# Kernel optimization log

Measured on AMD Instinct MI355X. Metric: run time of the kernel, lower is better.

The kernel has to match this reference:

```python
import jax, jax.numpy as jnp
import numpy as np

N, E, D, EH, EF, NT, OUT = 100000, 320000, 32, 32, 16, 100, 3
NUM_STEPS = 3


def setup_inputs() -> dict:
    key = jax.random.key(0)
    ks = iter(jax.random.split(key, 40))
    def rn(shape, s=0.1):
        return jax.random.normal(next(ks), shape, dtype=jnp.float32) * s
    return {
        "nfeats": jax.random.randint(next(ks), (N, 1), 0, NT),
        "efeats": jax.random.normal(next(ks), (E, EF), dtype=jnp.float32),
        "src": jax.random.randint(next(ks), (E,), 0, N, dtype=jnp.int32),
        "dst": jax.random.randint(next(ks), (E,), 0, N, dtype=jnp.int32),
        "emb_table": rn((NT, D), 1.0),
        "enc_W": rn((D, D)), "enc_b": rn((D,)),
        "eenc_W": rn((EF, EH)), "eenc_b": rn((EH,)),
        "proj_W": rn((D, D)), "proj_b": rn((D,)),
        "en_W1": rn((EH, EH)), "en_b1": rn((EH,)),
        "en_W2": rn((EH, D * D), 0.05), "en_b2": rn((D * D,), 0.05),
        "conv_b": rn((D,)),
        "gru_Wi": rn((D, 3 * D)), "gru_Wh": rn((D, 3 * D)),
        "gru_bi": rn((3 * D,)), "gru_bh": rn((3 * D,)),
        "dec_W1": rn((D, D)), "dec_b1": rn((D,)), "dec_a1": jnp.float32(0.25),
        "dec_W2": rn((D, D)), "dec_b2": rn((D,)), "dec_a2": jnp.float32(0.25),
        "dec_W3": rn((D, D)), "dec_b3": rn((D,)), "dec_a3": jnp.float32(0.25),
        "dec_W4": rn((D, OUT)), "dec_b4": rn((OUT,)),
    }


def _prelu(x, a):
    return jnp.where(x >= 0, x, a * x)


def reference(nfeats, efeats, src, dst, emb_table, enc_W, enc_b, eenc_W, eenc_b,
              proj_W, proj_b, en_W1, en_b1, en_W2, en_b2, conv_b,
              gru_Wi, gru_Wh, gru_bi, gru_bh,
              dec_W1, dec_b1, dec_a1, dec_W2, dec_b2, dec_a2,
              dec_W3, dec_b3, dec_a3, dec_W4, dec_b4):
    d = proj_W.shape[1]
    n = nfeats.shape[0]
    ntypes = nfeats.squeeze(1)  # [N]
    # node encoder: Embedding -> ReLU -> Linear -> ReLU
    nh = jax.nn.relu(jax.nn.relu(emb_table[ntypes]) @ enc_W + enc_b)  # [N, D]
    # edge encoder: Linear(efeat_dim, 32)
    eh = efeats @ eenc_W + eenc_b  # [E, EH]
    # MPNNGNN: project node feats
    h = jax.nn.relu(nh @ proj_W + proj_b)  # [N, D]
    # NNConv edge network: per-edge D x D weight matrix (identical every step)
    We = (jax.nn.relu(eh @ en_W1 + en_b1) @ en_W2 + en_b2).reshape(-1, d, d)  # [E, D, D]
    for _ in range(NUM_STEPS):
        # gather -> per-edge matvec -> scatter-sum to dst
        msg = jnp.einsum('ei,eio->eo', h[src], We)  # [E, D]
        agg = jax.ops.segment_sum(msg, dst, num_segments=n) + conv_b  # [N, D]
        x = jax.nn.relu(agg)
        # single GRU step (PyTorch gate order: r, z, n)
        gi = x @ gru_Wi + gru_bi
        gh = h @ gru_Wh + gru_bh
        ir, iz, inn = jnp.split(gi, 3, axis=-1)
        hr, hz, hn = jnp.split(gh, 3, axis=-1)
        r = jax.nn.sigmoid(ir + hr)
        z = jax.nn.sigmoid(iz + hz)
        ng = jnp.tanh(inn + r * hn)
        h = (1.0 - z) * ng + z * h
    y = _prelu(h @ dec_W1 + dec_b1, dec_a1)
    y = _prelu(y @ dec_W2 + dec_b2, dec_a2)
    y = _prelu(y @ dec_W3 + dec_b3, dec_a3)
    return y @ dec_W4 + dec_b4  # [N, OUT]
```

## Files before the change

### kernel.cpp

```cpp
#include <hip/hip_runtime.h>
#include <hip/hip_bf16.h>


#define NN 100000
#define NE 320000
#define QC 1056
#define NTS 6250
#define NT_D 3125
#define HB 256
#define EPB (NE / HB)
#define QSTRH 1072

typedef short bf16x8 __attribute__((ext_vector_type(8)));
typedef float f32x4  __attribute__((ext_vector_type(4)));

__device__ __forceinline__ float bf2f(unsigned short u) {
    return __uint_as_float(((unsigned int)u) << 16);
}
__device__ __forceinline__ unsigned short f2bf(float f) {
    unsigned int x = __float_as_uint(f);
    unsigned int r = (x + 0x7fffu + ((x >> 16) & 1u)) >> 16;
    return (unsigned short)r;
}
__device__ __forceinline__ float sigm(float x) {
    return 1.f / (1.f + __expf(-x));
}

__global__ __launch_bounds__(256) void k_w2ext(const float* __restrict__ W2,
                                               const float* __restrict__ b2,
                                               float* __restrict__ W2ext) {
    int idx = blockIdx.x * 256 + threadIdx.x;
    if (idx >= 32 * QC) return;
    int i = idx / QC, c = idx % QC;
    float v;
    if (c < 1024) { int k = c >> 5, o = c & 31; v = W2[k * 1024 + i * 32 + o]; }
    else          { v = b2[i * 32 + (c - 1024)]; }
    W2ext[idx] = v;
}

__global__ __launch_bounds__(256) void k_prepAll(
    const float* __restrict__ W2, const float* __restrict__ b2,
    unsigned short* __restrict__ W2bf,
    const float* __restrict__ Wi, const float* __restrict__ Wh,
    unsigned short* __restrict__ Whi, unsigned short* __restrict__ Wlo,
    const float* __restrict__ eencW, const float* __restrict__ eencB,
    const float* __restrict__ enW1, const float* __restrict__ enB1,
    float* __restrict__ Wcomb, float* __restrict__ bcomb) {
    int idx = blockIdx.x * 256 + threadIdx.x;
    if (idx < 66 * 512) {
        int ct = idx >> 9, l = (idx >> 3) & 63, j = idx & 7;
        int kk = ((j >> 2) << 4) + ((l >> 4) << 2) + (j & 3);
        int c = ct * 16 + (l & 15);
        float v;
        if (c < 1024) { int kb = c >> 5, o = c & 31; v = W2[kb * 1024 + kk * 32 + o]; }
        else          { v = b2[kk * 32 + (c - 1024)]; }
        W2bf[idx] = f2bf(v);
    } else if (idx < 66 * 512 + 6144) {
        int q = idx - 66 * 512;
        int j = q & 7, l = (q >> 3) & 63, kt = (q >> 9) & 1, nt = q >> 10;
        int k = ((j >> 2) << 4) + ((l >> 4) << 2) + (j & 3);
        int col = nt * 16 + (l & 15);
        float v = kt ? Wh[k * 96 + col] : Wi[k * 96 + col];
        unsigned short hi = f2bf(v);
        Whi[q] = hi;
        Wlo[q] = f2bf(v - bf2f(hi));
    } else if (idx < 66 * 512 + 6144 + 544) {
        int q = idx - 66 * 512 - 6144;
        if (q < 512) {
            int i = q >> 5, o = q & 31;
            float acc = 0.f;
            #pragma unroll 8
            for (int j = 0; j < 32; ++j) acc += eencW[i * 32 + j] * enW1[j * 32 + o];
            Wcomb[i * 32 + o] = acc;
        } else {
            int o = q - 512;
            float acc = enB1[o];
            #pragma unroll 8
            for (int j = 0; j < 32; ++j) acc += eencB[j] * enW1[j * 32 + o];
            bcomb[o] = acc;
        }
    }
}

__global__ __launch_bounds__(256) void k_histB(const int* __restrict__ src,
                                               const int* __restrict__ dst,
                                               int* __restrict__ bcS,
                                               int* __restrict__ bcD) {
    __shared__ int sHist[NTS];
    int tid = threadIdx.x, b = blockIdx.x;
    bool isS = b < HB;
    int bb = isS ? b : b - HB;
    const int* keys = isS ? src : dst;
    int NT = isS ? NTS : NT_D;
    int SH = isS ? 4 : 5;
    for (int c = tid; c < NT; c += 256) sHist[c] = 0;
    __syncthreads();
    int beg = bb * EPB, end = min(beg + EPB, NE);
    for (int e = beg + tid; e < end; e += 256)
        atomicAdd(&sHist[keys[e] >> SH], 1);
    __syncthreads();
    int* out = isS ? bcS : bcD;
    for (int c = tid; c < NT; c += 256) out[bb * NT + c] = sHist[c];
}

__global__ __launch_bounds__(256) void k_colsumB(const int* __restrict__ bcS,
                                                 const int* __restrict__ bcD,
                                                 int* __restrict__ bsS,
                                                 int* __restrict__ bsD,
                                                 int* __restrict__ totS,
                                                 int* __restrict__ totD) {
    int c = blockIdx.x * 256 + threadIdx.x;
    if (c < NTS) {
        int running = 0;
        #pragma unroll 8
        for (int b = 0; b < HB; ++b) {
            bsS[b * NTS + c] = running;
            running += bcS[b * NTS + c];
        }
        totS[c] = running;
    } else if (c < NTS + NT_D) {
        int cc = c - NTS;
        int running = 0;
        #pragma unroll 8
        for (int b = 0; b < HB; ++b) {
            bsD[b * NT_D + cc] = running;
            running += bcD[b * NT_D + cc];
        }
        totD[cc] = running;
    }
}

__global__ __launch_bounds__(256) void k_scanB(const int* __restrict__ totS,
                                               const int* __restrict__ totD,
                                               int* __restrict__ offS,
                                               int* __restrict__ offD) {
    __shared__ int sTot[NTS];
    __shared__ int sPart[257];
    int tid = threadIdx.x;
    const int* tot = (blockIdx.x == 0) ? totS : totD;
    int* offs = (blockIdx.x == 0) ? offS : offD;
    int NT = (blockIdx.x == 0) ? NTS : NT_D;
    int SEG = (blockIdx.x == 0) ? 25 : 13;
    for (int c = tid; c < NT; c += 256) sTot[c] = tot[c];
    __syncthreads();
    int base = tid * SEG;
    int loc = 0;
    for (int j = 0; j < SEG; ++j) {
        int c = base + j;
        if (c < NT) { int v = sTot[c]; sTot[c] = loc; loc += v; }
    }
    sPart[tid] = loc;
    __syncthreads();
    if (tid == 0) {
        int s = 0;
        for (int i = 0; i < 256; ++i) { int v = sPart[i]; sPart[i] = s; s += v; }
        sPart[256] = s;
    }
    __syncthreads();
    int add = sPart[tid];
    for (int j = 0; j < SEG; ++j) {
        int c = base + j;
        if (c < NT) sTot[c] += add;
    }
    __syncthreads();
    for (int c = tid; c < NT; c += 256) offs[c] = sTot[c];
    if (tid == 0) offs[NT] = sPart[256];
}

__global__ __launch_bounds__(256) void k_scatterB(const int* __restrict__ src,
                                                  const int* __restrict__ dst,
                                                  const int* __restrict__ bsS,
                                                  const int* __restrict__ bsD,
                                                  const int* __restrict__ offS,
                                                  const int* __restrict__ offD,
                                                  int* __restrict__ epS,
                                                  int* __restrict__ epD) {
    __shared__ int sCur[NTS];
    int tid = threadIdx.x, b = blockIdx.x;
    bool isS = b < HB;
    int bb = isS ? b : b - HB;
    const int* keys = isS ? src : dst;
    const int* bs = isS ? bsS : bsD;
    const int* offs = isS ? offS : offD;
    int* ep = isS ? epS : epD;
    int NT = isS ? NTS : NT_D;
    int SH = isS ? 4 : 5;
    for (int c = tid; c < NT; c += 256)
        sCur[c] = offs[c] + bs[bb * NT + c];
    __syncthreads();
    int beg = bb * EPB, end = min(beg + EPB, NE);
    for (int e = beg + tid; e < end; e += 256) {
        int pos = atomicAdd(&sCur[keys[e] >> SH], 1);
        ep[pos] = e;
    }
}

__global__ __launch_bounds__(256) void k_invgather(const int* __restrict__ epermS,
                                                   const int* __restrict__ src,
                                                   int* __restrict__ posS,
                                                   int* __restrict__ srcS) {
    int p = blockIdx.x * 256 + threadIdx.x;
    if (p < NE) {
        int e = epermS[p];
        posS[e] = p;
        srcS[p] = src[e];
    }
}

__global__ __launch_bounds__(256) void k_node_enc(
    const int* __restrict__ nfeats, const float* __restrict__ emb,
    const float* __restrict__ encW, const float* __restrict__ encB,
    const float* __restrict__ projW, const float* __restrict__ projB,
    float* __restrict__ h) {
    __shared__ float sEncW[1024], sProjW[1024], sEncB[32], sProjB[32];
    __shared__ float sEmb[8][33], sNh[8][33];
    int tid = threadIdx.x;
    for (int i = tid; i < 1024; i += 256) { sEncW[i] = encW[i]; sProjW[i] = projW[i]; }
    if (tid < 32) { sEncB[tid] = encB[tid]; sProjB[tid] = projB[tid]; }
    int ln = tid >> 5, o = tid & 31;
    int node = blockIdx.x * 8 + ln;
    int nt = nfeats[node];
    sEmb[ln][o] = fmaxf(emb[nt * 32 + o], 0.f);
    __syncthreads();
    float acc = sEncB[o];
    #pragma unroll
    for (int i = 0; i < 32; ++i) acc += sEmb[ln][i] * sEncW[i * 32 + o];
    sNh[ln][o] = fmaxf(acc, 0.f);
    __syncthreads();
    float acc2 = sProjB[o];
    #pragma unroll
    for (int i = 0; i < 32; ++i) acc2 += sNh[ln][i] * sProjW[i * 32 + o];
    h[node * 32 + o] = fmaxf(acc2, 0.f);
}

__global__ __launch_bounds__(256) void k_edge_t3(
    const float* __restrict__ efeats, const float* __restrict__ Wcomb,
    const float* __restrict__ bcomb, const int* __restrict__ eperm,
    float* __restrict__ tS) {
    int tid = threadIdx.x;
    int el = tid >> 3, l8 = tid & 7;
    int gbase = (tid & 63) & 56;
    int c0 = l8 << 2;
    float4 w[16];
    #pragma unroll
    for (int i = 0; i < 16; ++i) w[i] = *(const float4*)(Wcomb + i * 32 + c0);
    float4 bb = *(const float4*)(bcomb + c0);
    #pragma unroll
    for (int it = 0; it < 4; ++it) {
        int p = blockIdx.x * 128 + it * 32 + el;
        int e = eperm ? eperm[p] : p;
        float2 efv = *(const float2*)(efeats + (size_t)e * 16 + (l8 << 1));
        float a0 = bb.x, a1 = bb.y, a2 = bb.z, a3 = bb.w;
        #pragma unroll
        for (int i = 0; i < 8; ++i) {
            float f0 = __shfl(efv.x, gbase + i, 64);
            float f1 = __shfl(efv.y, gbase + i, 64);
            float4 w0 = w[2 * i], w1 = w[2 * i + 1];
            a0 += f0 * w0.x + f1 * w1.x;
            a1 += f0 * w0.y + f1 * w1.y;
            a2 += f0 * w0.z + f1 * w1.z;
            a3 += f0 * w0.w + f1 * w1.w;
        }
        *(float4*)(tS + (size_t)p * 32 + c0) =
            make_float4(fmaxf(a0, 0.f), fmaxf(a1, 0.f), fmaxf(a2, 0.f), fmaxf(a3, 0.f));
    }
}

template<int NT, int SHIFT>
__global__ __launch_bounds__(256) void k_histT(const int* __restrict__ keys,
                                               int* __restrict__ blockCounts) {
    __shared__ int sHist[NT];
    int tid = threadIdx.x, b = blockIdx.x;
    for (int c = tid; c < NT; c += 256) sHist[c] = 0;
    __syncthreads();
    int beg = b * EPB, end = min(beg + EPB, NE);
    for (int e = beg + tid; e < end; e += 256)
        atomicAdd(&sHist[keys[e] >> SHIFT], 1);
    __syncthreads();
    for (int c = tid; c < NT; c += 256) blockCounts[b * NT + c] = sHist[c];
}

template<int NT>
__global__ __launch_bounds__(256) void k_colsumT(const int* __restrict__ blockCounts,
                                                 int* __restrict__ blockStart,
                                                 int* __restrict__ tileTot) {
    int c = blockIdx.x * 256 + threadIdx.x;
    if (c >= NT) return;
    int running = 0;
    #pragma unroll 8
    for (int b = 0; b < HB; ++b) {
        blockStart[b * NT + c] = running;
        running += blockCounts[b * NT + c];
    }
    tileTot[c] = running;
}

template<int NT, int SEG>
__global__ __launch_bounds__(256) void k_scanT(const int* __restrict__ tileTot,
                                               int* __restrict__ offs) {
    __shared__ int sTot[NT];
    __shared__ int sPart[257];
    int tid = threadIdx.x;
    for (int c = tid; c < NT; c += 256) sTot[c] = tileTot[c];
    __syncthreads();
    int base = tid * SEG;
    int loc = 0;
    for (int j = 0; j < SEG; ++j) {
        int c = base + j;
        if (c < NT) { int v = sTot[c]; sTot[c] = loc; loc += v; }
    }
    sPart[tid] = loc;
    __syncthreads();
    if (tid == 0) {
        int s = 0;
        for (int i = 0; i < 256; ++i) { int v = sPart[i]; sPart[i] = s; s += v; }
        sPart[256] = s;
    }
    __syncthreads();
    int add = sPart[tid];
    for (int j = 0; j < SEG; ++j) {
        int c = base + j;
        if (c < NT) sTot[c] += add;
    }
    __syncthreads();
    for (int c = tid; c < NT; c += 256) offs[c] = sTot[c];
    if (tid == 0) offs[NT] = sPart[256];
}

template<int NT, int SHIFT>
__global__ __launch_bounds__(256) void k_scatterT(const int* __restrict__ keys,
                                                  const int* __restrict__ blockStart,
                                                  const int* __restrict__ offs,
                                                  int* __restrict__ eperm) {
    __shared__ int sCur[NT];
    int tid = threadIdx.x, b = blockIdx.x;
    for (int c = tid; c < NT; c += 256)
        sCur[c] = offs[c] + blockStart[b * NT + c];
    __syncthreads();
    int beg = b * EPB, end = min(beg + EPB, NE);
    for (int e = beg + tid; e < end; e += 256) {
        int pos = atomicAdd(&sCur[keys[e] >> SHIFT], 1);
        eperm[pos] = e;
    }
}

__global__ __launch_bounds__(256) void k_sortNode(
    const int* __restrict__ epermD, const int* __restrict__ dst,
    const int* __restrict__ offsD, int* __restrict__ epermD2,
    int* __restrict__ nodeOffs) {
    __shared__ int sCnt[32], sStart[32];
    int tid = threadIdx.x, d = blockIdx.x;
    int beg = offsD[d], end = offsD[d + 1];
    if (tid < 32) sCnt[tid] = 0;
    __syncthreads();
    for (int p = beg + tid; p < end; p += 256)
        atomicAdd(&sCnt[dst[epermD[p]] & 31], 1);
    __syncthreads();
    if (tid == 0) {
        int s = beg;
        for (int r = 0; r < 32; ++r) { sStart[r] = s; s += sCnt[r]; }
    }
    __syncthreads();
    if (tid < 32) {
        nodeOffs[d * 32 + tid] = sStart[tid];
        sCnt[tid] = sStart[tid];
    }
    if (d == NT_D - 1 && tid == 0) nodeOffs[NN] = end;
    __syncthreads();
    for (int p = beg + tid; p < end; p += 256) {
        int e = epermD[p];
        int pos = atomicAdd(&sCnt[dst[e] & 31], 1);
        epermD2[pos] = e;
    }
}

__global__ __launch_bounds__(256) void k_invperm(const int* __restrict__ eperm,
                                                 int* __restrict__ pos) {
    int p = blockIdx.x * 256 + threadIdx.x;
    if (p < NE) pos[eperm[p]] = p;
}

__global__ __launch_bounds__(256) void k_gatherKey(const int* __restrict__ epermS,
                                                   const int* __restrict__ key,
                                                   int* __restrict__ out) {
    int p = blockIdx.x * 256 + threadIdx.x;
    if (p < NE) out[p] = key[epermS[p]];
}

__global__ __launch_bounds__(256) void k_scatterIdx(const int* __restrict__ epermD2,
                                                    const int* __restrict__ posS,
                                                    int* __restrict__ idxS) {
    int q = blockIdx.x * 256 + threadIdx.x;
    if (q < NE) idxS[posS[epermD2[q]]] = q;
}

template<int MODE>
__global__ __launch_bounds__(256) void k_msgF16(
    const float* __restrict__ h, const unsigned short* __restrict__ W2bf,
    const float* __restrict__ tS, const int* __restrict__ srcS,
    const int* __restrict__ idxS, const int* __restrict__ offs,
    float* __restrict__ outbuf) {
    __shared__ unsigned short sQ[16 * QSTRH];
    int tid = threadIdx.x;
    int tile = blockIdx.x;
    int beg = offs[tile], end = offs[tile + 1];
    if (beg >= end) return;
    int nodeBase = tile * 16;
    int wave = tid >> 6, lane = tid & 63;

    int arow = lane & 15;
    const float* hp = h + (size_t)(nodeBase + arow) * 32 + ((lane >> 4) << 2);
    float4 x0 = *(const float4*)hp;
    float4 x1 = *(const float4*)(hp + 16);
    bf16x8 a;
    a[0] = (short)f2bf(x0.x); a[1] = (short)f2bf(x0.y);
    a[2] = (short)f2bf(x0.z); a[3] = (short)f2bf(x0.w);
    a[4] = (short)f2bf(x1.x); a[5] = (short)f2bf(x1.y);
    a[6] = (short)f2bf(x1.z); a[7] = (short)f2bf(x1.w);

    f32x4 z = {0.f, 0.f, 0.f, 0.f};
    int crow0 = (lane >> 4) << 2;
    int ccol = lane & 15;
    for (int ct = wave; ct < 66; ct += 4) {
        bf16x8 b = *(const bf16x8*)(W2bf + (size_t)((ct << 6) + lane) * 8);
        f32x4 acc = __builtin_amdgcn_mfma_f32_16x16x32_bf16(a, b, z, 0, 0, 0);
        unsigned short* qp = sQ + crow0 * QSTRH + (ct << 4) + ccol;
        qp[0 * QSTRH] = f2bf(acc[0]); qp[1 * QSTRH] = f2bf(acc[1]);
        qp[2 * QSTRH] = f2bf(acc[2]); qp[3 * QSTRH] = f2bf(acc[3]);
    }
    __syncthreads();

    int el = tid >> 2, l4 = tid & 3;
    for (int p = beg + el; p < end; p += 64) {
        int row = srcS[p] - nodeBase;
        int widx = idxS[p];
        float4 tq[8];
        #pragma unroll
        for (int i = 0; i < 8; ++i)
            tq[i] = *(const float4*)(tS + (size_t)p * 32 + (i << 2));
        const unsigned short* qp = sQ + row * QSTRH + (l4 << 3);
        bf16x8 qb = *(const bf16x8*)(qp + 1024);
        float acc[8];
        #pragma unroll
        for (int j = 0; j < 8; ++j) acc[j] = bf2f((unsigned short)qb[j]);
        #pragma unroll
        for (int kk = 0; kk < 8; ++kk) {
            float tv[4] = {tq[kk].x, tq[kk].y, tq[kk].z, tq[kk].w};
            #pragma unroll
            for (int m = 0; m < 4; ++m) {
                bf16x8 q = *(const bf16x8*)(qp + ((kk << 2) + m) * 32);
                float tk = tv[m];
                #pragma unroll
                for (int j = 0; j < 8; ++j)
                    acc[j] += tk * bf2f((unsigned short)q[j]);
            }
        }
        if (MODE) {
            float* op = outbuf + (size_t)widx * 32 + (l4 << 3);
            *(float4*)op = make_float4(acc[0], acc[1], acc[2], acc[3]);
            *(float4*)(op + 4) = make_float4(acc[4], acc[5], acc[6], acc[7]);
        } else {
            float* op = outbuf + (size_t)widx * 32 + (l4 << 3);
            #pragma unroll
            for (int j = 0; j < 8; ++j) atomicAdd(op + j, acc[j]);
        }
    }
}

__global__ __launch_bounds__(256) void k_msgC(
    const float* __restrict__ t, const int* __restrict__ src, const int* __restrict__ dst,
    const float* __restrict__ h, const float* __restrict__ W2ext, float* __restrict__ agg) {
    __shared__ float sT[32][33], sH[32][33];
    __shared__ int sSrc[32], sDst[32];
    int tid = threadIdx.x;
    int e0 = blockIdx.x * 32;
    if (tid < 32) sSrc[tid] = src[e0 + tid];
    else if (tid < 64) sDst[tid - 32] = dst[e0 + tid - 32];
    __syncthreads();
    for (int idx = tid; idx < 1024; idx += 256) {
        int el = idx >> 5, k = idx & 31;
        sT[el][k] = t[(e0 + el) * 32 + k];
        sH[el][k] = h[(size_t)sSrc[el] * 32 + k];
    }
    __syncthreads();
    int el = tid >> 3, l8 = tid & 7;
    int c0 = l8 * 4;
    float m0 = 0.f, m1 = 0.f, m2 = 0.f, m3 = 0.f;
    for (int i = 0; i < 32; ++i) {
        const float* wrow = W2ext + i * QC;
        float4 wb = *(const float4*)(wrow + 1024 + c0);
        float w0 = wb.x, w1 = wb.y, w2 = wb.z, w3 = wb.w;
        #pragma unroll 8
        for (int k = 0; k < 32; ++k) {
            float tk = sT[el][k];
            float4 w = *(const float4*)(wrow + k * 32 + c0);
            w0 += tk * w.x; w1 += tk * w.y; w2 += tk * w.z; w3 += tk * w.w;
        }
        float hi = sH[el][i];
        m0 += hi * w0; m1 += hi * w1; m2 += hi * w2; m3 += hi * w3;
    }
    float* ap = agg + (size_t)sDst[el] * 32 + c0;
    atomicAdd(ap + 0, m0); atomicAdd(ap + 1, m1);
    atomicAdd(ap + 2, m2); atomicAdd(ap + 3, m3);
}

__global__ __launch_bounds__(256) void k_gru(
    const float* __restrict__ agg, const float* __restrict__ convB,
    const float* __restrict__ Wi, const float* __restrict__ Wh,
    const float* __restrict__ bi, const float* __restrict__ bh,
    float* __restrict__ h) {
    __shared__ float sWi[3072], sWh[3072], sBi[96], sBh[96], sCb[32];
    __shared__ float sX[8][33], sH[8][33];
    int tid = threadIdx.x;
    for (int i = tid; i < 3072; i += 256) { sWi[i] = Wi[i]; sWh[i] = Wh[i]; }
    if (tid < 96) { sBi[tid] = bi[tid]; sBh[tid] = bh[tid]; }
    if (tid < 32) sCb[tid] = convB[tid];
    int ln = tid >> 5, o = tid & 31;
    for (int g = 0; g < 4; ++g) {
        int node = blockIdx.x * 32 + g * 8 + ln;
        float hv = h[node * 32 + o];
        float av = agg[node * 32 + o];
        __syncthreads();
        sX[ln][o] = fmaxf(av + sCb[o], 0.f);
        sH[ln][o] = hv;
        __syncthreads();
        float air = sBi[o], aiz = sBi[o + 32], ain = sBi[o + 64];
        float ahr = sBh[o], ahz = sBh[o + 32], ahn = sBh[o + 64];
        #pragma unroll 8
        for (int i = 0; i < 32; ++i) {
            float x = sX[ln][i], hh = sH[ln][i];
            air += x * sWi[i * 96 + o];      ahr += hh * sWh[i * 96 + o];
            aiz += x * sWi[i * 96 + o + 32]; ahz += hh * sWh[i * 96 + o + 32];
            ain += x * sWi[i * 96 + o + 64]; ahn += hh * sWh[i * 96 + o + 64];
        }
        float r = sigm(air + ahr);
        float zz = sigm(aiz + ahz);
        float ng = tanhf(ain + r * ahn);
        h[node * 32 + o] = (1.f - zz) * ng + zz * hv;
    }
}

__global__ __launch_bounds__(256) void k_gruAgg4(
    const float* __restrict__ msgbuf, const int* __restrict__ nodeOffs,
    const float* __restrict__ convB,
    const unsigned short* __restrict__ Whi, const unsigned short* __restrict__ Wlo,
    const float* __restrict__ bi, const float* __restrict__ bh,
    float* __restrict__ h) {
    __shared__ float sAgg[32 * 33];
    int tid = threadIdx.x;
    int d = blockIdx.x;
    int base = d * 32;

    {
        int n8 = tid >> 3, l8 = tid & 7;
        int node = base + n8;
        int nb = nodeOffs[node], ne2 = nodeOffs[node + 1];
        float a0 = 0.f, a1 = 0.f, a2 = 0.f, a3 = 0.f;
        for (int p = nb; p < ne2; ++p) {
            float4 v = *(const float4*)(msgbuf + (size_t)p * 32 + (l8 << 2));
            a0 += v.x; a1 += v.y; a2 += v.z; a3 += v.w;
        }
        int c0 = l8 << 2;
        float4 cb = *(const float4*)(convB + c0);
        float* sp = sAgg + n8 * 33 + c0;
        sp[0] = fmaxf(a0 + cb.x, 0.f);
        sp[1] = fmaxf(a1 + cb.y, 0.f);
        sp[2] = fmaxf(a2 + cb.z, 0.f);
        sp[3] = fmaxf(a3 + cb.w, 0.f);
    }
    __syncthreads();

    int wave = tid >> 6, lane = tid & 63;
    int m = wave >> 1, c = wave & 1;
    int arow = lane & 15, kg = (lane >> 4) << 2;

    bf16x8 xhi, xlo, hhi, hlo;
    {
        const float* xp = sAgg + (m * 16 + arow) * 33 + kg;
        float4 v0 = *(const float4*)xp;
        float4 v1 = *(const float4*)(xp + 16);
        float xv[8] = {v0.x, v0.y, v0.z, v0.w, v1.x, v1.y, v1.z, v1.w};
        #pragma unroll
        for (int j = 0; j < 8; ++j) {
            unsigned short hi16 = f2bf(xv[j]);
            xhi[j] = (short)hi16;
            xlo[j] = (short)f2bf(xv[j] - bf2f(hi16));
        }
        const float* hp = h + (size_t)(base + m * 16 + arow) * 32 + kg;
        float4 w0 = *(const float4*)hp;
        float4 w1 = *(const float4*)(hp + 16);
        float hv8[8] = {w0.x, w0.y, w0.z, w0.w, w1.x, w1.y, w1.z, w1.w};
        #pragma unroll
        for (int j = 0; j < 8; ++j) {
            unsigned short hi16 = f2bf(hv8[j]);
            hhi[j] = (short)hi16;
            hlo[j] = (short)f2bf(hv8[j] - bf2f(hi16));
        }
    }

    int ccol = lane & 15, crow0 = (lane >> 4) << 2;
    int o = c * 16 + ccol;
    auto Bf = [&](int nt, int kt, const unsigned short* W) {
        return *(const bf16x8*)(W + (size_t)(((nt * 2 + kt) * 64 + lane) << 3));
    };
    f32x4 accR = {0.f, 0.f, 0.f, 0.f}, accZ = {0.f, 0.f, 0.f, 0.f};
    f32x4 accIN = {0.f, 0.f, 0.f, 0.f}, accHN = {0.f, 0.f, 0.f, 0.f};
    {
        int nt = c;
        bf16x8 b0h = Bf(nt, 0, Whi), b0l = Bf(nt, 0, Wlo);
        bf16x8 b1h = Bf(nt, 1, Whi), b1l = Bf(nt, 1, Wlo);
        accR = __builtin_amdgcn_mfma_f32_16x16x32_bf16(xhi, b0h, accR, 0, 0, 0);
        accR = __builtin_amdgcn_mfma_f32_16x16x32_bf16(xlo, b0h, accR, 0, 0, 0);
        accR = __builtin_amdgcn_mfma_f32_16x16x32_bf16(xhi, b0l, accR, 0, 0, 0);
        accR = __builtin_amdgcn_mfma_f32_16x16x32_bf16(hhi, b1h, accR, 0, 0, 0);
        accR = __builtin_amdgcn_mfma_f32_16x16x32_bf16(hlo, b1h, accR, 0, 0, 0);
        accR = __builtin_amdgcn_mfma_f32_16x16x32_bf16(hhi, b1l, accR, 0, 0, 0);
    }
    {
        int nt = 2 + c;
        bf16x8 b0h = Bf(nt, 0, Whi), b0l = Bf(nt, 0, Wlo);
        bf16x8 b1h = Bf(nt, 1, Whi), b1l = Bf(nt, 1, Wlo);
        accZ = __builtin_amdgcn_mfma_f32_16x16x32_bf16(xhi, b0h, accZ, 0, 0, 0);
        accZ = __builtin_amdgcn_mfma_f32_16x16x32_bf16(xlo, b0h, accZ, 0, 0, 0);
        accZ = __builtin_amdgcn_mfma_f32_16x16x32_bf16(xhi, b0l, accZ, 0, 0, 0);
        accZ = __builtin_amdgcn_mfma_f32_16x16x32_bf16(hhi, b1h, accZ, 0, 0, 0);
        accZ = __builtin_amdgcn_mfma_f32_16x16x32_bf16(hlo, b1h, accZ, 0, 0, 0);
        accZ = __builtin_amdgcn_mfma_f32_16x16x32_bf16(hhi, b1l, accZ, 0, 0, 0);
    }
    {
        int nt = 4 + c;
        bf16x8 b0h = Bf(nt, 0, Whi), b0l = Bf(nt, 0, Wlo);
        bf16x8 b1h = Bf(nt, 1, Whi), b1l = Bf(nt, 1, Wlo);
        accIN = __builtin_amdgcn_mfma_f32_16x16x32_bf16(xhi, b0h, accIN, 0, 0, 0);
        accIN = __builtin_amdgcn_mfma_f32_16x16x32_bf16(xlo, b0h, accIN, 0, 0, 0);
        accIN = __builtin_amdgcn_mfma_f32_16x16x32_bf16(xhi, b0l, accIN, 0, 0, 0);
        accHN = __builtin_amdgcn_mfma_f32_16x16x32_bf16(hhi, b1h, accHN, 0, 0, 0);
        accHN = __builtin_amdgcn_mfma_f32_16x16x32_bf16(hlo, b1h, accHN, 0, 0, 0);
        accHN = __builtin_amdgcn_mfma_f32_16x16x32_bf16(hhi, b1l, accHN, 0, 0, 0);
    }

    float bir = bi[o], biz = bi[32 + o], bin = bi[64 + o];
    float bhr = bh[o], bhz = bh[32 + o], bhn = bh[64 + o];
    float hv[4];
    #pragma unroll
    for (int j = 0; j < 4; ++j)
        hv[j] = h[(size_t)(base + m * 16 + crow0 + j) * 32 + o];
    __syncthreads();
    #pragma unroll
    for (int j = 0; j < 4; ++j) {
        float r  = sigm(accR[j] + bir + bhr);
        float zz = sigm(accZ[j] + biz + bhz);
        float ng = tanhf(accIN[j] + bin + r * (accHN[j] + bhn));
        h[(size_t)(base + m * 16 + crow0 + j) * 32 + o] = (1.f - zz) * ng + zz * hv[j];
    }
}

__global__ __launch_bounds__(256) void k_dec(
    const float* __restrict__ h,
    const float* __restrict__ W1, const float* __restrict__ b1, const float* __restrict__ a1,
    const float* __restrict__ W2, const float* __restrict__ b2, const float* __restrict__ a2,
    const float* __restrict__ W3, const float* __restrict__ b3, const float* __restrict__ a3,
    const float* __restrict__ W4, const float* __restrict__ b4,
    float* __restrict__ out) {
    __shared__ float sW1[1024], sW2[1024], sW3[1024], sW4[96];
    __shared__ float sB1[32], sB2[32], sB3[32], sB4[3];
    __shared__ float sYa[8][33], sYb[8][33];
    int tid = threadIdx.x;
    for (int i = tid; i < 1024; i += 256) { sW1[i] = W1[i]; sW2[i] = W2[i]; sW3[i] = W3[i]; }
    if (tid < 96) sW4[tid] = W4[tid];
    if (tid < 32) { sB1[tid] = b1[tid]; sB2[tid] = b2[tid]; sB3[tid] = b3[tid]; }
    if (tid < 3) sB4[tid] = b4[tid];
    float A1 = a1[0], A2 = a2[0], A3 = a3[0];
    int ln = tid >> 5, o = tid & 31;
    int node = blockIdx.x * 8 + ln;
    sYa[ln][o] = h[node * 32 + o];
    __syncthreads();
    float acc = sB1[o];
    #pragma unroll
    for (int i = 0; i < 32; ++i) acc += sYa[ln][i] * sW1[i * 32 + o];
    acc = acc >= 0.f ? acc : A1 * acc;
    sYb[ln][o] = acc;
    __syncthreads();
    acc = sB2[o];
    #pragma unroll
    for (int i = 0; i < 32; ++i) acc += sYb[ln][i] * sW2[i * 32 + o];
    acc = acc >= 0.f ? acc : A2 * acc;
    __syncthreads();
    sYa[ln][o] = acc;
    __syncthreads();
    acc = sB3[o];
    #pragma unroll
    for (int i = 0; i < 32; ++i) acc += sYa[ln][i] * sW3[i * 32 + o];
    acc = acc >= 0.f ? acc : A3 * acc;
    __syncthreads();
    sYb[ln][o] = acc;
    __syncthreads();
    if (o < 3) {
        float r = sB4[o];
        #pragma unroll
        for (int i = 0; i < 32; ++i) r += sYb[ln][i] * sW4[i * 3 + o];
        out[node * 3 + o] = r;
    }
}

extern "C" void kernel_launch(void* const* d_in, const int* in_sizes, int n_in,
                              void* d_out, int out_size, void* d_ws, size_t ws_size,
                              hipStream_t stream) {
    const int*   nfeats = (const int*)d_in[0];
    const float* efeats = (const float*)d_in[1];
    const int*   src    = (const int*)d_in[2];
    const int*   dst    = (const int*)d_in[3];
    const float* emb    = (const float*)d_in[4];
    const float* encW   = (const float*)d_in[5];
    const float* encB   = (const float*)d_in[6];
    const float* eencW  = (const float*)d_in[7];
    const float* eencB  = (const float*)d_in[8];
    const float* projW  = (const float*)d_in[9];
    const float* projB  = (const float*)d_in[10];
    const float* enW1   = (const float*)d_in[11];
    const float* enB1   = (const float*)d_in[12];
    const float* enW2   = (const float*)d_in[13];
    const float* enB2   = (const float*)d_in[14];
    const float* convB  = (const float*)d_in[15];
    const float* gruWi  = (const float*)d_in[16];
    const float* gruWh  = (const float*)d_in[17];
    const float* gruBi  = (const float*)d_in[18];
    const float* gruBh  = (const float*)d_in[19];
    const float* dW1 = (const float*)d_in[20]; const float* db1 = (const float*)d_in[21]; const float* da1 = (const float*)d_in[22];
    const float* dW2 = (const float*)d_in[23]; const float* db2 = (const float*)d_in[24]; const float* da2 = (const float*)d_in[25];
    const float* dW3 = (const float*)d_in[26]; const float* db3 = (const float*)d_in[27]; const float* da3 = (const float*)d_in[28];
    const float* dW4 = (const float*)d_in[29]; const float* db4 = (const float*)d_in[30];
    float* out = (float*)d_out;
    char* ws = (char*)d_ws;

    size_t cur = 0;
    auto alloc = [&](size_t n) { size_t p = cur; cur = (cur + n + 255) & ~(size_t)255; return p; };
    size_t o_h   = alloc((size_t)NN * 32 * 4);
    size_t o_t   = alloc((size_t)NE * 32 * 4);
    size_t o_w2e = alloc((size_t)32 * QC * 4);
    size_t afterCommon = cur;
    size_t o_w2b = alloc((size_t)66 * 512 * 2);
    size_t o_epS = alloc((size_t)NE * 4);
    size_t o_ofS = alloc((size_t)(NTS + 1) * 4);
    size_t o_posS = alloc((size_t)NE * 4);
    size_t o_srcS = alloc((size_t)NE * 4);
    size_t o_idxS = alloc((size_t)NE * 4);
    size_t o_wcomb = alloc((size_t)(512 + 32) * 4);
    size_t baseEnd = cur;
    size_t o_epD  = alloc((size_t)NE * 4);
    size_t o_ofD  = alloc((size_t)(NT_D + 1) * 4);
    size_t o_epD2 = alloc((size_t)NE * 4);
    size_t o_noff = alloc((size_t)(NN + 1) * 4);
    size_t o_whi  = alloc((size_t)6144 * 2);
    size_t o_wlo  = alloc((size_t)6144 * 2);
    size_t o_msg  = alloc((size_t)NE * 32 * 4);
    size_t need1 = cur;
    size_t need0 = baseEnd + (size_t)NN * 32 * 4;

    int mode;
    if (ws_size >= need1) mode = 1;
    else if (ws_size >= need0) mode = 0;
    else mode = -1;

    float* h     = (float*)(ws + o_h);
    float* tS    = (float*)(ws + o_t);
    float* W2ext = (float*)(ws + o_w2e);
    unsigned short* W2bf = (unsigned short*)(ws + o_w2b);
    int* epermS  = (int*)(ws + o_epS);
    int* offsS   = (int*)(ws + o_ofS);
    int* posS    = (int*)(ws + o_posS);
    int* srcS    = (int*)(ws + o_srcS);
    int* idxS    = (int*)(ws + o_idxS);
    float* Wcomb = (float*)(ws + o_wcomb);
    float* bcomb = Wcomb + 512;
    int* epermD  = (int*)(ws + o_epD);
    int* offsD   = (int*)(ws + o_ofD);
    int* epermD2 = (int*)(ws + o_epD2);
    int* nodeOffs = (int*)(ws + o_noff);
    unsigned short* gWhi = (unsigned short*)(ws + o_whi);
    unsigned short* gWlo = (unsigned short*)(ws + o_wlo);
    float* outbuf = (mode == 1) ? (float*)(ws + o_msg)
                  : (mode == 0) ? (float*)(ws + baseEnd)
                                : (float*)(ws + afterCommon);
    int* bcS = (int*)outbuf;
    int* bsS = bcS + (size_t)HB * NTS;
    int* bcD = bsS + (size_t)HB * NTS;
    int* bsD = bcD + (size_t)HB * NT_D;
    int* totS = bsD + (size_t)HB * NT_D;
    int* totD = totS + NTS;

    k_node_enc<<<NN / 8, 256, 0, stream>>>(nfeats, emb, encW, encB, projW, projB, h);

    if (mode == 1) {
        k_prepAll<<<(66 * 512 + 6144 + 544 + 255) / 256, 256, 0, stream>>>(
            enW2, enB2, W2bf, gruWi, gruWh, gWhi, gWlo,
            eencW, eencB, enW1, enB1, Wcomb, bcomb);
        k_histB<<<2 * HB, 256, 0, stream>>>(src, dst, bcS, bcD);
        k_colsumB<<<(NTS + NT_D + 255) / 256, 256, 0, stream>>>(bcS, bcD, bsS, bsD, totS, totD);
        k_scanB<<<2, 256, 0, stream>>>(totS, totD, offsS, offsD);
        k_scatterB<<<2 * HB, 256, 0, stream>>>(src, dst, bsS, bsD, offsS, offsD, epermS, epermD);
        k_invgather<<<(NE + 255) / 256, 256, 0, stream>>>(epermS, src, posS, srcS);
        k_sortNode<<<NT_D, 256, 0, stream>>>(epermD, dst, offsD, epermD2, nodeOffs);
        k_scatterIdx<<<(NE + 255) / 256, 256, 0, stream>>>(epermD2, posS, idxS);
        k_edge_t3<<<NE / 128, 256, 0, stream>>>(efeats, Wcomb, bcomb, epermS, tS);
    } else if (mode == 0) {
        int* blockCounts = (int*)outbuf;
        int* blockStart  = blockCounts + (size_t)HB * NTS;
        int* tileTot     = blockStart + (size_t)HB * NTS;
        k_prepAll<<<(66 * 512 + 6144 + 544 + 255) / 256, 256, 0, stream>>>(
            enW2, enB2, W2bf, gruWi, gruWh, gWhi, gWlo,
            eencW, eencB, enW1, enB1, Wcomb, bcomb);
        k_histT<NTS, 4><<<HB, 256, 0, stream>>>(src, blockCounts);
        k_colsumT<NTS><<<(NTS + 255) / 256, 256, 0, stream>>>(blockCounts, blockStart, tileTot);
        k_scanT<NTS, 25><<<1, 256, 0, stream>>>(tileTot, offsS);
        k_scatterT<NTS, 4><<<HB, 256, 0, stream>>>(src, blockStart, offsS, epermS);
        k_invperm<<<(NE + 255) / 256, 256, 0, stream>>>(epermS, posS);
        k_gatherKey<<<(NE + 255) / 256, 256, 0, stream>>>(epermS, src, srcS);
        k_gatherKey<<<(NE + 255) / 256, 256, 0, stream>>>(epermS, dst, idxS);
        k_edge_t3<<<NE / 128, 256, 0, stream>>>(efeats, Wcomb, bcomb, epermS, tS);
    } else {
        k_prepAll<<<(66 * 512 + 6144 + 544 + 255) / 256, 256, 0, stream>>>(
            enW2, enB2, W2bf, gruWi, gruWh, gWhi, gWlo,
            eencW, eencB, enW1, enB1, Wcomb, bcomb);
        k_w2ext<<<(32 * QC + 255) / 256, 256, 0, stream>>>(enW2, enB2, W2ext);
        k_edge_t3<<<NE / 128, 256, 0, stream>>>(efeats, Wcomb, bcomb, nullptr, tS);
    }

    for (int s = 0; s < 3; ++s) {
        if (mode == 1) {
            k_msgF16<1><<<NTS, 256, 0, stream>>>(h, W2bf, tS, srcS, idxS, offsS, outbuf);
            k_gruAgg4<<<NT_D, 256, 0, stream>>>(outbuf, nodeOffs, convB,
                                                gWhi, gWlo, gruBi, gruBh, h);
        } else if (mode == 0) {
            hipMemsetAsync(outbuf, 0, (size_t)NN * 32 * 4, stream);
            k_msgF16<0><<<NTS, 256, 0, stream>>>(h, W2bf, tS, srcS, idxS, offsS, outbuf);
            k_gru<<<NN / 32, 256, 0, stream>>>(outbuf, convB, gruWi, gruWh, gruBi, gruBh, h);
        } else {
            hipMemsetAsync(outbuf, 0, (size_t)NN * 32 * 4, stream);
            k_msgC<<<NE / 32, 256, 0, stream>>>(tS, src, dst, h, W2ext, outbuf);
            k_gru<<<NN / 32, 256, 0, stream>>>(outbuf, convB, gruWi, gruWh, gruBi, gruBh, h);
        }
    }
    k_dec<<<NN / 8, 256, 0, stream>>>(h, dW1, db1, da1, dW2, db2, da2, dW3, db3, da3, dW4, db4, out);
}
```

Before: 414.0 us.

## Store edge hidden features and per-tile Q in fp16, use packed dot2 accumulation

The per-edge hidden vectors tS are now written as fp16 instead of fp32, which halves the per-edge read traffic in the message kernel on every step. The shared-memory Q tile is stored as fp16 with k-pairs interleaved. This lets the inner contraction use packed fp16 dot2 instructions instead of converting bf16 to fp32 and running scalar FMAs. The tradeoff is fp16 range and precision on the activations, plus an extra index computation when Q is written to shared memory.

```diff
diff --git a/kernel.cpp b/kernel.cpp
--- a/kernel.cpp
+++ b/kernel.cpp
@@ -13,6 +13,8 @@
 
 typedef short bf16x8 __attribute__((ext_vector_type(8)));
 typedef float f32x4  __attribute__((ext_vector_type(4)));
+typedef _Float16 h16x2 __attribute__((ext_vector_type(2)));
+typedef _Float16 h16x8 __attribute__((ext_vector_type(8)));
 
 __device__ __forceinline__ float bf2f(unsigned short u) {
     return __uint_as_float(((unsigned int)u) << 16);
@@ -24,6 +26,13 @@
 }
 __device__ __forceinline__ float sigm(float x) {
     return 1.f / (1.f + __expf(-x));
+}
+__device__ __forceinline__ float dot2h(h16x2 a, h16x2 b, float c) {
+#if __has_builtin(__builtin_amdgcn_fdot2)
+    return __builtin_amdgcn_fdot2(a, b, c, false);
+#else
+    return c + (float)a[0] * (float)b[0] + (float)a[1] * (float)b[1];
+#endif
 }
 
 __global__ __launch_bounds__(256) void k_w2ext(const float* __restrict__ W2,
@@ -233,10 +242,10 @@
     h[node * 32 + o] = fmaxf(acc2, 0.f);
 }
 
-__global__ __launch_bounds__(256) void k_edge_t3(
+__global__ __launch_bounds__(256) void k_edge_t3h(
     const float* __restrict__ efeats, const float* __restrict__ Wcomb,
     const float* __restrict__ bcomb, const int* __restrict__ eperm,
-    float* __restrict__ tS) {
+    unsigned short* __restrict__ tS) {
     int tid = threadIdx.x;
     int el = tid >> 3, l8 = tid & 7;
     int gbase = (tid & 63) & 56;
@@ -261,6 +270,45 @@
             a2 += f0 * w0.z + f1 * w1.z;
             a3 += f0 * w0.w + f1 * w1.w;
         }
+        _Float16 h0 = (_Float16)fmaxf(a0, 0.f);
+        _Float16 h1 = (_Float16)fmaxf(a1, 0.f);
+        _Float16 h2 = (_Float16)fmaxf(a2, 0.f);
+        _Float16 h3 = (_Float16)fmaxf(a3, 0.f);
+        ushort4 o4;
+        o4.x = *(unsigned short*)&h0; o4.y = *(unsigned short*)&h1;
+        o4.z = *(unsigned short*)&h2; o4.w = *(unsigned short*)&h3;
+        *(ushort4*)(tS + (size_t)p * 32 + c0) = o4;
+    }
+}
+
+__global__ __launch_bounds__(256) void k_edge_t3(
+    const float* __restrict__ efeats, const float* __restrict__ Wcomb,
+    const float* __restrict__ bcomb, const int* __restrict__ eperm,
+    float* __restrict__ tS) {
+    int tid = threadIdx.x;
+    int el = tid >> 3, l8 = tid & 7;
+    int gbase = (tid & 63) & 56;
+    int c0 = l8 << 2;
+    float4 w[16];
+    #pragma unroll
+    for (int i = 0; i < 16; ++i) w[i] = *(const float4*)(Wcomb + i * 32 + c0);
+    float4 bb = *(const float4*)(bcomb + c0);
+    #pragma unroll
+    for (int it = 0; it < 4; ++it) {
+        int p = blockIdx.x * 128 + it * 32 + el;
+        int e = eperm ? eperm[p] : p;
+        float2 efv = *(const float2*)(efeats + (size_t)e * 16 + (l8 << 1));
+        float a0 = bb.x, a1 = bb.y, a2 = bb.z, a3 = bb.w;
+        #pragma unroll
+        for (int i = 0; i < 8; ++i) {
+            float f0 = __shfl(efv.x, gbase + i, 64);
+            float f1 = __shfl(efv.y, gbase + i, 64);
+            float4 w0 = w[2 * i], w1 = w[2 * i + 1];
+            a0 += f0 * w0.x + f1 * w1.x;
+            a1 += f0 * w0.y + f1 * w1.y;
+            a2 += f0 * w0.z + f1 * w1.z;
+            a3 += f0 * w0.w + f1 * w1.w;
+        }
         *(float4*)(tS + (size_t)p * 32 + c0) =
             make_float4(fmaxf(a0, 0.f), fmaxf(a1, 0.f), fmaxf(a2, 0.f), fmaxf(a3, 0.f));
     }
@@ -397,7 +445,7 @@
 template<int MODE>
 __global__ __launch_bounds__(256) void k_msgF16(
     const float* __restrict__ h, const unsigned short* __restrict__ W2bf,
-    const float* __restrict__ tS, const int* __restrict__ srcS,
+    const unsigned short* __restrict__ tS, const int* __restrict__ srcS,
     const int* __restrict__ idxS, const int* __restrict__ offs,
     float* __restrict__ outbuf) {
     __shared__ unsigned short sQ[16 * QSTRH];
@@ -424,43 +472,59 @@
     for (int ct = wave; ct < 66; ct += 4) {
         bf16x8 b = *(const bf16x8*)(W2bf + (size_t)((ct << 6) + lane) * 8);
         f32x4 acc = __builtin_amdgcn_mfma_f32_16x16x32_bf16(a, b, z, 0, 0, 0);
-        unsigned short* qp = sQ + crow0 * QSTRH + (ct << 4) + ccol;
-        qp[0 * QSTRH] = f2bf(acc[0]); qp[1 * QSTRH] = f2bf(acc[1]);
-        qp[2 * QSTRH] = f2bf(acc[2]); qp[3 * QSTRH] = f2bf(acc[3]);
+        int c = (ct << 4) + ccol;
+        int idx;
+        if (c < 1024) {
+            int k = c >> 5, o = c & 31;
+            idx = ((k >> 1) << 6) + (o << 1) + (k & 1);
+        } else {
+            idx = 1024 + (c - 1024);
+        }
+        unsigned short* qp = sQ + crow0 * QSTRH + idx;
+        _Float16 v0 = (_Float16)acc[0], v1 = (_Float16)acc[1];
+        _Float16 v2 = (_Float16)acc[2], v3 = (_Float16)acc[3];
+        qp[0 * QSTRH] = *(unsigned short*)&v0;
+        qp[1 * QSTRH] = *(unsigned short*)&v1;
+        qp[2 * QSTRH] = *(unsigned short*)&v2;
+        qp[3 * QSTRH] = *(unsigned short*)&v3;
     }
     __syncthreads();
 
     int el = tid >> 2, l4 = tid & 3;
+    int o0 = l4 << 3;
     for (int p = beg + el; p < end; p += 64) {
         int row = srcS[p] - nodeBase;
         int widx = idxS[p];
-        float4 tq[8];
+        h16x8 trow[4];
         #pragma unroll
-        for (int i = 0; i < 8; ++i)
-            tq[i] = *(const float4*)(tS + (size_t)p * 32 + (i << 2));
-        const unsigned short* qp = sQ + row * QSTRH + (l4 << 3);
-        bf16x8 qb = *(const bf16x8*)(qp + 1024);
+        for (int i = 0; i < 4; ++i)
+            trow[i] = *(const h16x8*)(tS + (size_t)p * 32 + (i << 3));
+        const unsigned short* qp = sQ + row * QSTRH;
+        h16x8 qb = *(const h16x8*)(qp + 1024 + o0);
         float acc[8];
         #pragma unroll
-        for (int j = 0; j < 8; ++j) acc[j] = bf2f((unsigned short)qb[j]);
+        for (int j = 0; j < 8; ++j) acc[j] = (float)qb[j];
         #pragma unroll
-        for (int kk = 0; kk < 8; ++kk) {
-            float tv[4] = {tq[kk].x, tq[kk].y, tq[kk].z, tq[kk].w};
+        for (int kp = 0; kp < 16; ++kp) {
+            h16x2 t2;
+            t2[0] = trow[kp >> 2][(kp & 3) * 2];
+            t2[1] = trow[kp >> 2][(kp & 3) * 2 + 1];
+            h16x8 qa = *(const h16x8*)(qp + (kp << 6) + (o0 << 1));
+            h16x8 qc = *(const h16x8*)(qp + (kp << 6) + (o0 << 1) + 8);
             #pragma unroll
-            for (int m = 0; m < 4; ++m) {
-                bf16x8 q = *(const bf16x8*)(qp + ((kk << 2) + m) * 32);
-                float tk = tv[m];
-                #pragma unroll
-                for (int j = 0; j < 8; ++j)
-                    acc[j] += tk * bf2f((unsigned short)q[j]);
+            for (int j = 0; j < 4; ++j) {
+                h16x2 q2a; q2a[0] = qa[2 * j]; q2a[1] = qa[2 * j + 1];
+                h16x2 q2c; q2c[0] = qc[2 * j]; q2c[1] = qc[2 * j + 1];
+                acc[j]     = dot2h(t2, q2a, acc[j]);
+                acc[4 + j] = dot2h(t2, q2c, acc[4 + j]);
             }
         }
         if (MODE) {
-            float* op = outbuf + (size_t)widx * 32 + (l4 << 3);
+            float* op = outbuf + (size_t)widx * 32 + o0;
             *(float4*)op = make_float4(acc[0], acc[1], acc[2], acc[3]);
             *(float4*)(op + 4) = make_float4(acc[4], acc[5], acc[6], acc[7]);
         } else {
-            float* op = outbuf + (size_t)widx * 32 + (l4 << 3);
+            float* op = outbuf + (size_t)widx * 32 + o0;
             #pragma unroll
             for (int j = 0; j < 8; ++j) atomicAdd(op + j, acc[j]);
         }
@@ -763,7 +827,8 @@
     else mode = -1;
 
     float* h     = (float*)(ws + o_h);
-    float* tS    = (float*)(ws + o_t);
+    float* tSf   = (float*)(ws + o_t);
+    unsigned short* tSh = (unsigned short*)(ws + o_t);
     float* W2ext = (float*)(ws + o_w2e);
     unsigned short* W2bf = (unsigned short*)(ws + o_w2b);
     int* epermS  = (int*)(ws + o_epS);
@@ -802,7 +867,7 @@
         k_invgather<<<(NE + 255) / 256, 256, 0, stream>>>(epermS, src, posS, srcS);
         k_sortNode<<<NT_D, 256, 0, stream>>>(epermD, dst, offsD, epermD2, nodeOffs);
         k_scatterIdx<<<(NE + 255) / 256, 256, 0, stream>>>(epermD2, posS, idxS);
-        k_edge_t3<<<NE / 128, 256, 0, stream>>>(efeats, Wcomb, bcomb, epermS, tS);
+        k_edge_t3h<<<NE / 128, 256, 0, stream>>>(efeats, Wcomb, bcomb, epermS, tSh);
     } else if (mode == 0) {
         int* blockCounts = (int*)outbuf;
         int* blockStart  = blockCounts + (size_t)HB * NTS;
@@ -817,27 +882,27 @@
         k_invperm<<<(NE + 255) / 256, 256, 0, stream>>>(epermS, posS);
         k_gatherKey<<<(NE + 255) / 256, 256, 0, stream>>>(epermS, src, srcS);
         k_gatherKey<<<(NE + 255) / 256, 256, 0, stream>>>(epermS, dst, idxS);
-        k_edge_t3<<<NE / 128, 256, 0, stream>>>(efeats, Wcomb, bcomb, epermS, tS);
+        k_edge_t3h<<<NE / 128, 256, 0, stream>>>(efeats, Wcomb, bcomb, epermS, tSh);
     } else {
         k_prepAll<<<(66 * 512 + 6144 + 544 + 255) / 256, 256, 0, stream>>>(
             enW2, enB2, W2bf, gruWi, gruWh, gWhi, gWlo,
             eencW, eencB, enW1, enB1, Wcomb, bcomb);
         k_w2ext<<<(32 * QC + 255) / 256, 256, 0, stream>>>(enW2, enB2, W2ext);
-        k_edge_t3<<<NE / 128, 256, 0, stream>>>(efeats, Wcomb, bcomb, nullptr, tS);
+        k_edge_t3<<<NE / 128, 256, 0, stream>>>(efeats, Wcomb, bcomb, nullptr, tSf);
     }
 
     for (int s = 0; s < 3; ++s) {
         if (mode == 1) {
-            k_msgF16<1><<<NTS, 256, 0, stream>>>(h, W2bf, tS, srcS, idxS, offsS, outbuf);
+            k_msgF16<1><<<NTS, 256, 0, stream>>>(h, W2bf, tSh, srcS, idxS, offsS, outbuf);
             k_gruAgg4<<<NT_D, 256, 0, stream>>>(outbuf, nodeOffs, convB,
                                                 gWhi, gWlo, gruBi, gruBh, h);
         } else if (mode == 0) {
             hipMemsetAsync(outbuf, 0, (size_t)NN * 32 * 4, stream);
-            k_msgF16<0><<<NTS, 256, 0, stream>>>(h, W2bf, tS, srcS, idxS, offsS, outbuf);
+            k_msgF16<0><<<NTS, 256, 0, stream>>>(h, W2bf, tSh, srcS, idxS, offsS, outbuf);
             k_gru<<<NN / 32, 256, 0, stream>>>(outbuf, convB, gruWi, gruWh, gruBi, gruBh, h);
         } else {
             hipMemsetAsync(outbuf, 0, (size_t)NN * 32 * 4, stream);
-            k_msgC<<<NE / 32, 256, 0, stream>>>(tS, src, dst, h, W2ext, outbuf);
+            k_msgC<<<NE / 32, 256, 0, stream>>>(tSf, src, dst, h, W2ext, outbuf);
             k_gru<<<NN / 32, 256, 0, stream>>>(outbuf, convB, gruWi, gruWh, gruBi, gruBh, h);
         }
     }
```

Measured after the change: 394.4 us. 4.7% less time.
